# Performance work log

Measured on AMD Instinct MI355X. Metric: run time of the kernel, lower is better.

The kernel has to match this reference:

```python
import jax, jax.numpy as jnp
import numpy as np

N = 20000
E = 320000
F_IN = 50
HID = 64          # hidden_channels
HEADS = 8
WIDTH = HID * HEADS  # 512
NUM_CLASSES = 121


def setup_inputs() -> dict:
    key = jax.random.key(0)
    ks = jax.random.split(key, 16)
    def p(k, shape, fan_in):
        return (jax.random.normal(k, shape, dtype=jnp.float32) / np.sqrt(fan_in)).astype(jnp.float32)
    x = jax.random.normal(ks[0], (N, F_IN), dtype=jnp.float32)
    edge_index = jax.random.randint(ks[1], (2, E), 0, N, dtype=jnp.int64)
    return {
        "x": x,
        "edge_index": edge_index,
        # layer 1: 50 -> 64, heads=8, concat
        "W1": p(ks[2], (F_IN, HEADS * HID), F_IN),
        "a1_src": p(ks[3], (HEADS, HID), HID),
        "a1_dst": p(ks[4], (HEADS, HID), HID),
        "b1": jnp.zeros((HEADS * HID,), jnp.float32),
        # layer 2: 512 -> 512, heads=1, concat
        "W2": p(ks[5], (WIDTH, WIDTH), WIDTH),
        "a2_src": p(ks[6], (1, WIDTH), WIDTH),
        "a2_dst": p(ks[7], (1, WIDTH), WIDTH),
        "b2": jnp.zeros((WIDTH,), jnp.float32),
        # layer 3: 512 -> 121, heads=1, concat=False (mean)
        "W3": p(ks[8], (WIDTH, NUM_CLASSES), WIDTH),
        "a3_src": p(ks[9], (1, NUM_CLASSES), NUM_CLASSES),
        "a3_dst": p(ks[10], (1, NUM_CLASSES), NUM_CLASSES),
        "b3": jnp.zeros((NUM_CLASSES,), jnp.float32),
    }


def gat_conv(x, src, dst, W, a_src, a_dst, b, heads, out_ch, concat):
    n = x.shape[0]
    h = (x @ W).reshape(n, heads, out_ch)                 # [N, H, C]
    al_s = jnp.sum(h * a_src, axis=-1)                     # [N, H]
    al_d = jnp.sum(h * a_dst, axis=-1)                     # [N, H]
    e = jax.nn.leaky_relu(al_s[src] + al_d[dst], 0.2)      # [E, H]
    # edge softmax per destination node (stable)
    m = jax.ops.segment_max(e, dst, num_segments=n)        # [N, H]
    m = jnp.where(jnp.isfinite(m), m, 0.0)
    ex = jnp.exp(e - m[dst])
    z = jax.ops.segment_sum(ex, dst, num_segments=n)       # [N, H]
    alpha = ex / (z[dst] + 1e-16)                          # [E, H]
    msg = h[src] * alpha[..., None]                        # [E, H, C]
    out = jax.ops.segment_sum(msg, dst, num_segments=n)    # [N, H, C]
    out = out.reshape(n, heads * out_ch) if concat else out.mean(axis=1)
    return out + b


def reference(x, edge_index, W1, a1_src, a1_dst, b1, W2, a2_src, a2_dst, b2, W3, a3_src, a3_dst, b3):
    n = x.shape[0]
    # PyG GATConv adds self loops by default
    loops = jnp.arange(n, dtype=edge_index.dtype)
    src = jnp.concatenate([edge_index[0], loops])
    dst = jnp.concatenate([edge_index[1], loops])
    # eval mode: dropout is identity
    x1 = gat_conv(x, src, dst, W1, a1_src, a1_dst, b1, HEADS, HID, True)
    h = jax.nn.elu(x1)
    x1 = gat_conv(h, src, dst, W2, a2_src, a2_dst, b2, 1, WIDTH, True)
    h = jax.nn.elu(x1)
    x1 = gat_conv(h, src, dst, W3, a3_src, a3_dst, b3, 1, NUM_CLASSES, False)
    return x1
```

## Files before the change

### kernel.cpp

```cpp
#include <hip/hip_runtime.h>
#include <hip/hip_bf16.h>
#include <hip/hip_fp16.h>

#define NN     20000
#define ERAW   320000
#define ETOT   (ERAW + NN)
#define F_IN   50
#define HID    64
#define HEADS  8
#define WIDTH  512
#define NCLS   121
#define NCLS_P 128

typedef __attribute__((ext_vector_type(8))) __bf16 bf16x8;
typedef __attribute__((ext_vector_type(4))) float floatx4;

__device__ __forceinline__ unsigned short f32_to_bf16_rn(float f) {
  unsigned u = __float_as_uint(f);
  unsigned r = u + 0x7fffu + ((u >> 16) & 1u);
  return (unsigned short)(r >> 16);
}
__device__ __forceinline__ void split_one(float f, unsigned short& h,
                                          unsigned short& l) {
  h = f32_to_bf16_rn(f);
  float fh = __uint_as_float(((unsigned)h) << 16);
  l = f32_to_bf16_rn(f - fh);
}

__device__ __forceinline__ float2 u2f2(unsigned u) {
  __half2 hv = *reinterpret_cast<__half2*>(&u);
  return __half22float2(hv);
}

__device__ __forceinline__ void gll16(const unsigned short* g,
                                      const unsigned short* l) {
  __builtin_amdgcn_global_load_lds(
      (const __attribute__((address_space(1))) unsigned int*)(const void*)g,
      (__attribute__((address_space(3))) unsigned int*)(void*)l, 16, 0, 0);
}

#define PW_BLOCKS 449
__global__ __launch_bounds__(256) void prep_weights(
    const float* __restrict__ W1, const float* __restrict__ W2,
    const float* __restrict__ W3, const float* __restrict__ a1s,
    const float* __restrict__ a1d, unsigned short* __restrict__ w1hHi,
    unsigned short* __restrict__ w1hLo, unsigned short* __restrict__ w2tHi,
    unsigned short* __restrict__ w2tLo, unsigned short* __restrict__ w3tHi,
    unsigned short* __restrict__ w3tLo, float* __restrict__ w1as,
    float* __restrict__ w1ad) {
  __shared__ float t[32][33];
  const int b = blockIdx.x;
  if (b < 320) {
    const float* W;
    unsigned short *thi, *tlo;
    int M, Mp, bx, by;
    const int K = WIDTH;
    if (b < 256) {
      W = W2; thi = w2tHi; tlo = w2tLo; M = WIDTH; Mp = WIDTH;
      bx = b & 15; by = b >> 4;
    } else {
      int bb = b - 256;
      W = W3; thi = w3tHi; tlo = w3tLo; M = NCLS; Mp = NCLS_P;
      bx = bb & 15; by = bb >> 4;
    }
    const int P = Mp >> 4;
    int k0 = bx * 32, m0 = by * 32;
    int tx = threadIdx.x & 31, ty = threadIdx.x >> 5;
    #pragma unroll
    for (int r = 0; r < 4; ++r) {
      int k = k0 + ty + r * 8, m = m0 + tx;
      float v = 0.f;
      if (k < K && m < M) v = W[(size_t)k * M + m];
      t[ty + r * 8][tx] = v;
    }
    __syncthreads();
    #pragma unroll
    for (int r = 0; r < 4; ++r) {
      int m = m0 + ty + r * 8, k = k0 + tx;
      if (m < Mp && k < K) {
        unsigned short h, l;
        split_one(t[tx][ty + r * 8], h, l);
        size_t off = ((size_t)((k >> 5) * P + (m >> 4))) * 512 +
                     ((k >> 3) & 3) * 128 + (m & 15) * 8 + (k & 7);
        thi[off] = h;
        tlo[off] = l;
      }
    }
  } else if (b < 448) {
    int idx = (b - 320) * 256 + threadIdx.x;
    if (idx < HEADS * HID * HID) {
      int hd = idx >> 12, rem = idx & 4095;
      int col = rem >> 6, k = rem & 63;
      float v = (k < F_IN) ? W1[(size_t)k * WIDTH + hd * HID + col] : 0.f;
      unsigned short h, l;
      split_one(v, h, l);
      w1hHi[idx] = h;
      w1hLo[idx] = l;
    }
  } else {
    for (int idx = threadIdx.x; idx < 2 * F_IN * HEADS; idx += 256) {
      int which = idx >= F_IN * HEADS;
      int r = which ? idx - F_IN * HEADS : idx;
      int k = r >> 3, h = r & 7;
      const float* a = which ? a1d : a1s;
      float s = 0.f;
      for (int c = 0; c < HID; ++c)
        s += W1[(size_t)k * WIDTH + h * HID + c] * a[h * HID + c];
      (which ? w1ad : w1as)[r] = s;
    }
  }
}

template <int MI>
__global__ __launch_bounds__(512, 4) void gemm_split_db(
    const unsigned short* __restrict__ Ahi, const unsigned short* __restrict__ Alo,
    const unsigned short* __restrict__ Bthi, const unsigned short* __restrict__ Btlo,
    __half* __restrict__ C16, int N, int K, int M, int Mp, int RB, int CB) {
  constexpr int ABUF = MI * 2048;
  constexpr int BUF = MI * 4096;
  constexpr int NGW = MI;
  __shared__ unsigned short lds[2 * BUF];

  const int f = blockIdx.x;
  const int xcd = f & 7;
  const int g = f >> 3;
  const int cb = g % CB;
  const int rb = (g / CB) * 8 + xcd;
  if (rb >= RB) return;
  const int r0 = rb * (MI * 32), c0 = cb * 128;

  const int tid = threadIdx.x;
  const int wave = tid >> 6, lane = tid & 63;
  const int wr = wave >> 2, wc = wave & 3;
  const int lkg = lane >> 4, lmn = lane & 15;
  const int P = Mp >> 4;

  const int row8 = lane >> 3, cslot = lane & 7;
  const unsigned short* gsrc[NGW];
  int ldsoff[NGW];
  #pragma unroll
  for (int i = 0; i < NGW; ++i) {
    int q = wave * NGW + i;
    int a = (q < MI * 4) ? 0 : 1;
    int rg = (a == 0) ? q : q - MI * 4;
    int r = rg * 8 + row8;
    int c = cslot ^ (r & 7);
    const unsigned short* base = a ? Alo : Ahi;
    int ra = r0 + r;
    if (ra > N - 1) ra = N - 1;
    gsrc[i] = base + (size_t)ra * K + c * 8;
    ldsoff[i] = a * ABUF + rg * 512;
  }

  int rowA[MI], m7A[MI];
  #pragma unroll
  for (int mi = 0; mi < MI; ++mi) {
    int m = wr * (MI * 16) + mi * 16 + lmn;
    rowA[mi] = m * 64;  m7A[mi] = m & 7;
  }
  const int g0 = (c0 >> 4) + wc * 2;

  floatx4 acc[MI][2] = {};

  #pragma unroll
  for (int i = 0; i < NGW; ++i) gll16(gsrc[i], lds + ldsoff[i]);

  const int nk = K >> 6;
  for (int t = 0; t < nk; ++t) {
    if (t + 1 < nk) {
      const unsigned short* dst = lds + ((t + 1) & 1) * BUF;
      #pragma unroll
      for (int i = 0; i < NGW; ++i)
        gll16(gsrc[i] + (t + 1) * 64, dst + ldsoff[i]);
      if constexpr (MI == 4) {
        asm volatile("s_waitcnt vmcnt(4)" ::: "memory");
      } else {
        asm volatile("s_waitcnt vmcnt(2)" ::: "memory");
      }
    } else {
      asm volatile("s_waitcnt vmcnt(0)" ::: "memory");
    }
    __builtin_amdgcn_sched_barrier(0);
    __builtin_amdgcn_s_barrier();
    __builtin_amdgcn_sched_barrier(0);

    const unsigned short* Lb = lds + (t & 1) * BUF;
    #pragma unroll
    for (int ksub = 0; ksub < 2; ++ksub) {
      bf16x8 fAhi[MI], fAlo[MI], fBhi[2], fBlo[2];
      #pragma unroll
      for (int mi = 0; mi < MI; ++mi) {
        int s = rowA[mi] + (((ksub << 2) | lkg) ^ m7A[mi]) * 8;
        fAhi[mi] = *(const bf16x8*)(Lb + s);
        fAlo[mi] = *(const bf16x8*)(Lb + s + ABUF);
      }
      const size_t fbase = ((size_t)(t * 2 + ksub) * P + g0) * 512 + lane * 8;
      #pragma unroll
      for (int ni = 0; ni < 2; ++ni) {
        fBhi[ni] = *(const bf16x8*)(Bthi + fbase + ni * 512);
        fBlo[ni] = *(const bf16x8*)(Btlo + fbase + ni * 512);
      }
      #pragma unroll
      for (int mi = 0; mi < MI; ++mi)
        #pragma unroll
        for (int ni = 0; ni < 2; ++ni) {
          acc[mi][ni] = __builtin_amdgcn_mfma_f32_16x16x32_bf16(
              fAhi[mi], fBhi[ni], acc[mi][ni], 0, 0, 0);
          acc[mi][ni] = __builtin_amdgcn_mfma_f32_16x16x32_bf16(
              fAhi[mi], fBlo[ni], acc[mi][ni], 0, 0, 0);
          acc[mi][ni] = __builtin_amdgcn_mfma_f32_16x16x32_bf16(
              fAlo[mi], fBhi[ni], acc[mi][ni], 0, 0, 0);
        }
    }

    __builtin_amdgcn_sched_barrier(0);
    asm volatile("s_waitcnt lgkmcnt(0)" ::: "memory");
    __builtin_amdgcn_s_barrier();
    __builtin_amdgcn_sched_barrier(0);
  }

  #pragma unroll
  for (int mi = 0; mi < MI; ++mi) {
    #pragma unroll
    for (int r = 0; r < 4; ++r) {
      int grow = r0 + wr * (MI * 16) + mi * 16 + lkg * 4 + r;
      if (grow >= N) continue;
      #pragma unroll
      for (int ni = 0; ni < 2; ++ni) {
        int gcol = c0 + wc * 32 + ni * 16 + lmn;
        float v = (gcol < M) ? acc[mi][ni][r] : 0.f;
        C16[(size_t)grow * Mp + gcol] = __float2half(v);
      }
    }
  }
}

__global__ __launch_bounds__(256) void gemm_l1_heads(
    const unsigned short* __restrict__ Ahi, const unsigned short* __restrict__ Alo,
    const unsigned short* __restrict__ Bthi, const unsigned short* __restrict__ Btlo,
    unsigned short* __restrict__ outHi, unsigned short* __restrict__ outLo,
    const float* __restrict__ bias) {
  __shared__ unsigned short sAhi[8192], sAlo[8192], sBhi[4096], sBlo[4096];
  const int tid = threadIdx.x;
  const int wave = tid >> 6, lane = tid & 63;
  const int r0 = blockIdx.x * 128;
  const int hd = blockIdx.y;
  const int lkg = lane >> 4, lmn = lane & 15;

  #pragma unroll
  for (int t = 0; t < 4; ++t) {
    int cid = tid + t * 256;
    int row = cid >> 3, c = cid & 7;
    int gr = r0 + row; if (gr > NN - 1) gr = NN - 1;
    const size_t goff = (size_t)gr * WIDTH + hd * HID + c * 8;
    int loff = (((c >> 2) * 4 + (c & 3)) * 128 + row) * 8;
    *(uint4*)(sAhi + loff) = *(const uint4*)(Ahi + goff);
    *(uint4*)(sAlo + loff) = *(const uint4*)(Alo + goff);
  }
  #pragma unroll
  for (int t = 0; t < 2; ++t) {
    int cid = tid + t * 256;
    int col = cid >> 3, c = cid & 7;
    const size_t goff = (size_t)(hd * HID + col) * HID + c * 8;
    int loff = (((c >> 2) * 4 + (c & 3)) * 64 + col) * 8;
    *(uint4*)(sBhi + loff) = *(const uint4*)(Bthi + goff);
    *(uint4*)(sBlo + loff) = *(const uint4*)(Btlo + goff);
  }
  __syncthreads();

  floatx4 acc[2][4] = {};
  #pragma unroll
  for (int ks = 0; ks < 2; ++ks) {
    bf16x8 fAhi[2], fAlo[2], fBhi[4], fBlo[4];
    #pragma unroll
    for (int mi = 0; mi < 2; ++mi) {
      int m = wave * 32 + mi * 16 + lmn;
      int off = ((ks * 4 + lkg) * 128 + m) * 8;
      fAhi[mi] = *(const bf16x8*)(sAhi + off);
      fAlo[mi] = *(const bf16x8*)(sAlo + off);
    }
    #pragma unroll
    for (int ni = 0; ni < 4; ++ni) {
      int n = ni * 16 + lmn;
      int off = ((ks * 4 + lkg) * 64 + n) * 8;
      fBhi[ni] = *(const bf16x8*)(sBhi + off);
      fBlo[ni] = *(const bf16x8*)(sBlo + off);
    }
    #pragma unroll
    for (int mi = 0; mi < 2; ++mi)
      #pragma unroll
      for (int ni = 0; ni < 4; ++ni) {
        acc[mi][ni] = __builtin_amdgcn_mfma_f32_16x16x32_bf16(
            fAhi[mi], fBhi[ni], acc[mi][ni], 0, 0, 0);
        acc[mi][ni] = __builtin_amdgcn_mfma_f32_16x16x32_bf16(
            fAhi[mi], fBlo[ni], acc[mi][ni], 0, 0, 0);
        acc[mi][ni] = __builtin_amdgcn_mfma_f32_16x16x32_bf16(
            fAlo[mi], fBhi[ni], acc[mi][ni], 0, 0, 0);
      }
  }

  #pragma unroll
  for (int mi = 0; mi < 2; ++mi) {
    #pragma unroll
    for (int r = 0; r < 4; ++r) {
      int grow = r0 + wave * 32 + mi * 16 + (lane >> 4) * 4 + r;
      if (grow >= NN) continue;
      #pragma unroll
      for (int ni = 0; ni < 4; ++ni) {
        int gcol = hd * HID + ni * 16 + lmn;
        float v = acc[mi][ni][r] + bias[gcol];
        v = (v > 0.f) ? v : (__expf(v) - 1.0f);
        unsigned short hh, ll;
        split_one(v, hh, ll);
        outHi[(size_t)grow * WIDTH + gcol] = hh;
        outLo[(size_t)grow * WIDTH + gcol] = ll;
      }
    }
  }
}

__global__ __launch_bounds__(256) void al1_kernel(
    const float* __restrict__ x, const float* __restrict__ w1as,
    const float* __restrict__ w1ad, float* __restrict__ al_s,
    float* __restrict__ al_d) {
  int n = (blockIdx.x * blockDim.x + threadIdx.x) >> 6;
  int lane = threadIdx.x & 63;
  if (n >= NN) return;
  float xv = (lane < F_IN) ? x[(size_t)n * F_IN + lane] : 0.f;
  float ws[HEADS], wd[HEADS];
  #pragma unroll
  for (int h = 0; h < HEADS; ++h) {
    ws[h] = (lane < F_IN) ? w1as[lane * HEADS + h] : 0.f;
    wd[h] = (lane < F_IN) ? w1ad[lane * HEADS + h] : 0.f;
  }
  #pragma unroll
  for (int h = 0; h < HEADS; ++h) {
    float ss = xv * ws[h], sd = xv * wd[h];
    #pragma unroll
    for (int o = 32; o; o >>= 1) {
      ss += __shfl_xor(ss, o);
      sd += __shfl_xor(sd, o);
    }
    if (lane == 0) {
      al_s[n * HEADS + h] = ss;
      al_d[n * HEADS + h] = sd;
    }
  }
}

template <int C, int CS>
__global__ __launch_bounds__(256) void compute_al16(
    const __half* __restrict__ h16, const float* __restrict__ a_src,
    const float* __restrict__ a_dst, float* __restrict__ al_s,
    float* __restrict__ al_d) {
  int n = (blockIdx.x * blockDim.x + threadIdx.x) >> 6;
  int lane = threadIdx.x & 63;
  if (n >= NN) return;
  const __half* hr = h16 + (size_t)n * CS;
  float ss = 0.f, sd = 0.f;
  if (C % 512 == 0) {
    uint4 raw = *(const uint4*)(hr + lane * 8);
    float f[8];
    float2 t;
    t = u2f2(raw.x); f[0] = t.x; f[1] = t.y;
    t = u2f2(raw.y); f[2] = t.x; f[3] = t.y;
    t = u2f2(raw.z); f[4] = t.x; f[5] = t.y;
    t = u2f2(raw.w); f[6] = t.x; f[7] = t.y;
    #pragma unroll
    for (int j = 0; j < 8; ++j) {
      int c = lane * 8 + j;
      ss += f[j] * a_src[c];
      sd += f[j] * a_dst[c];
    }
  } else {
    for (int c = lane; c < C; c += 64) {
      float v = __half2float(hr[c]);
      ss += v * a_src[c];
      sd += v * a_dst[c];
    }
  }
  #pragma unroll
  for (int o = 32; o; o >>= 1) {
    ss += __shfl_xor(ss, o);
    sd += __shfl_xor(sd, o);
  }
  if (lane == 0) {
    al_s[n] = ss;
    al_d[n] = sd;
  }
}

__global__ __launch_bounds__(256) void count_deg(
    const int* __restrict__ edst, int* __restrict__ deg) {
  int e = blockIdx.x * blockDim.x + threadIdx.x;
  if (e >= ETOT) return;
  int d = (e < ERAW) ? edst[e] : (e - ERAW);
  atomicAdd(&deg[d], 1);
}

__global__ __launch_bounds__(1024) void scan_deg(
    const int* __restrict__ deg, int* __restrict__ rowptr) {
  __shared__ int part[1024];
  const int t = threadIdx.x;
  const int CHUNK = (NN + 1023) / 1024;
  int lo = t * CHUNK, hi = min(lo + CHUNK, NN);
  int s = 0;
  for (int i = lo; i < hi; ++i) s += deg[i];
  part[t] = s;
  __syncthreads();
  for (int off = 1; off < 1024; off <<= 1) {
    int v = (t >= off) ? part[t - off] : 0;
    __syncthreads();
    part[t] += v;
    __syncthreads();
  }
  int base = (t == 0) ? 0 : part[t - 1];
  for (int i = lo; i < hi; ++i) {
    rowptr[i] = base;
    base += deg[i];
  }
  if (t == 1023) rowptr[NN] = part[1023];
}

__global__ __launch_bounds__(256) void scatter_csr(
    const int* __restrict__ esrc, const int* __restrict__ edst,
    const int* __restrict__ rowptr, int* __restrict__ cnt,
    int* __restrict__ csrc) {
  int e = blockIdx.x * blockDim.x + threadIdx.x;
  if (e >= ETOT) return;
  int s, d;
  if (e < ERAW) { s = esrc[e]; d = edst[e]; }
  else          { s = e - ERAW; d = e - ERAW; }
  int pos = rowptr[d] + atomicAdd(&cnt[d], 1);
  csrc[pos] = s;
}

__global__ __launch_bounds__(256) void agg_x_sm(
    const int* __restrict__ rowptr, const int* __restrict__ csrc,
    const float* __restrict__ al_s, const float* __restrict__ al_d,
    const float* __restrict__ x, unsigned short* __restrict__ outHi,
    unsigned short* __restrict__ outLo) {
  const int w = threadIdx.x >> 6, lane = threadIdx.x & 63;
  const int d = blockIdx.x * 4 + w;
  if (d >= NN) return;
  const int r0 = rowptr[d], r1 = rowptr[d + 1];
  const int mh = lane & 7;
  const float ald_my = al_d[d * HEADS + mh];
  float m_my = al_s[d * HEADS + mh] + ald_my;
  m_my = (m_my > 0.f) ? m_my : 0.2f * m_my;

  float z_my = 0.f;
  float acc[HEADS];
  #pragma unroll
  for (int hh = 0; hh < HEADS; ++hh) acc[hh] = 0.f;

  int p = r0;
  for (; p + 8 <= r1; p += 8) {
    int s[8];
    #pragma unroll
    for (int j = 0; j < 8; ++j) s[j] = csrc[p + j];
    float xv[8];
    #pragma unroll
    for (int j = 0; j < 8; ++j)
      xv[j] = (lane < F_IN) ? x[(size_t)s[j] * F_IN + lane] : 0.f;
    float av[8];
    #pragma unroll
    for (int j = 0; j < 8; ++j) av[j] = al_s[s[j] * HEADS + mh];
    #pragma unroll
    for (int j = 0; j < 8; ++j) {
      float v = av[j] + ald_my;
      v = (v > 0.f) ? v : 0.2f * v;
      float a = __expf(v - m_my);
      z_my += a;
      #pragma unroll
      for (int hh = 0; hh < HEADS; ++hh) acc[hh] += __shfl(a, hh, 8) * xv[j];
    }
  }
  for (; p < r1; ++p) {
    int s = csrc[p];
    float v = al_s[s * HEADS + mh] + ald_my;
    v = (v > 0.f) ? v : 0.2f * v;
    float a = __expf(v - m_my);
    z_my += a;
    float xv = (lane < F_IN) ? x[(size_t)s * F_IN + lane] : 0.f;
    #pragma unroll
    for (int hh = 0; hh < HEADS; ++hh) acc[hh] += __shfl(a, hh, 8) * xv;
  }

  #pragma unroll
  for (int hh = 0; hh < HEADS; ++hh) {
    float zh = __shfl(z_my, hh, 8);
    float v = (lane < F_IN) ? acc[hh] / (zh + 1e-16f) : 0.f;
    unsigned short h2, l2;
    split_one(v, h2, l2);
    outHi[(size_t)d * WIDTH + hh * HID + lane] = h2;
    outLo[(size_t)d * WIDTH + hh * HID + lane] = l2;
  }
}

__global__ __launch_bounds__(256) void pull_agg_w(
    const int* __restrict__ rowptr, const int* __restrict__ csrc,
    const float* __restrict__ al_s, const float* __restrict__ al_d,
    const __half* __restrict__ h16, const float* __restrict__ bias,
    unsigned short* __restrict__ outHi, unsigned short* __restrict__ outLo) {
  const int w = threadIdx.x >> 6;
  const int lane = threadIdx.x & 63;
  const int d = blockIdx.x * 4 + w;
  if (d >= NN) return;
  const int r0 = rowptr[d], r1 = rowptr[d + 1];
  const float ald = al_d[d];
  float m = al_s[d] + ald;
  m = (m > 0.f) ? m : 0.2f * m;

  const int base = lane * 8;
  const __half* hb = h16 + base;
  float acc[8];
  #pragma unroll
  for (int j = 0; j < 8; ++j) acc[j] = 0.f;
  float z = 0.f;

  int p = r0;
  for (; p + 8 <= r1; p += 8) {
    int s[8];
    #pragma unroll
    for (int j = 0; j < 8; ++j) s[j] = csrc[p + j];
    uint4 raw8[8];
    #pragma unroll
    for (int j = 0; j < 8; ++j)
      raw8[j] = *(const uint4*)(hb + (size_t)s[j] * WIDTH);
    float av[8];
    #pragma unroll
    for (int j = 0; j < 8; ++j) av[j] = al_s[s[j]];
    #pragma unroll
    for (int j = 0; j < 8; ++j) {
      float v = av[j] + ald;
      v = (v > 0.f) ? v : 0.2f * v;
      float a = __expf(v - m);
      z += a;
      float2 f0 = u2f2(raw8[j].x), f1 = u2f2(raw8[j].y);
      float2 f2 = u2f2(raw8[j].z), f3 = u2f2(raw8[j].w);
      acc[0] += f0.x * a; acc[1] += f0.y * a;
      acc[2] += f1.x * a; acc[3] += f1.y * a;
      acc[4] += f2.x * a; acc[5] += f2.y * a;
      acc[6] += f3.x * a; acc[7] += f3.y * a;
    }
  }
  for (; p < r1; ++p) {
    int s = csrc[p];
    float v = al_s[s] + ald;
    v = (v > 0.f) ? v : 0.2f * v;
    float a = __expf(v - m);
    z += a;
    uint4 raw = *(const uint4*)(hb + (size_t)s * WIDTH);
    float2 f0 = u2f2(raw.x), f1 = u2f2(raw.y);
    float2 f2 = u2f2(raw.z), f3 = u2f2(raw.w);
    acc[0] += f0.x * a; acc[1] += f0.y * a;
    acc[2] += f1.x * a; acc[3] += f1.y * a;
    acc[4] += f2.x * a; acc[5] += f2.y * a;
    acc[6] += f3.x * a; acc[7] += f3.y * a;
  }
  const float iz = 1.0f / (z + 1e-16f);

  #pragma unroll
  for (int j = 0; j < 8; ++j) {
    float v = acc[j] * iz + bias[base + j];
    v = (v > 0.f) ? v : (__expf(v) - 1.0f);
    unsigned short hh, ll;
    split_one(v, hh, ll);
    outHi[(size_t)d * WIDTH + base + j] = hh;
    outLo[(size_t)d * WIDTH + base + j] = ll;
  }
}

__global__ __launch_bounds__(256) void pull_agg_n(
    const int* __restrict__ rowptr, const int* __restrict__ csrc,
    const float* __restrict__ al_s, const float* __restrict__ al_d,
    const __half* __restrict__ h16, const float* __restrict__ bias,
    float* __restrict__ out) {
  const int w = threadIdx.x >> 6, lane = threadIdx.x & 63;
  const int half = lane >> 5, li = lane & 31;
  const int d = blockIdx.x * 8 + w * 2 + half;
  if (d >= NN) return;
  const int r0 = rowptr[d], r1 = rowptr[d + 1];
  const float ald = al_d[d];
  float m = al_s[d] + ald;
  m = (m > 0.f) ? m : 0.2f * m;

  const int base = li * 4;
  const __half* hb = h16 + base;
  float acc[4] = {0.f, 0.f, 0.f, 0.f};
  float z = 0.f;

  for (int p = r0; p < r1; p += 8) {
    int s[8];
    #pragma unroll
    for (int j = 0; j < 8; ++j) {
      int pj = p + j; if (pj > r1 - 1) pj = r1 - 1;
      s[j] = csrc[pj];
    }
    uint2 raw[8];
    #pragma unroll
    for (int j = 0; j < 8; ++j)
      raw[j] = *(const uint2*)(hb + (size_t)s[j] * NCLS_P);
    float av[8];
    #pragma unroll
    for (int j = 0; j < 8; ++j) av[j] = al_s[s[j]];
    #pragma unroll
    for (int j = 0; j < 8; ++j) {
      float v = av[j] + ald;
      v = (v > 0.f) ? v : 0.2f * v;
      float a = __expf(v - m);
      if (p + j >= r1) a = 0.f;
      z += a;
      float2 f0 = u2f2(raw[j].x), f1 = u2f2(raw[j].y);
      acc[0] += f0.x * a; acc[1] += f0.y * a;
      acc[2] += f1.x * a; acc[3] += f1.y * a;
    }
  }
  const float iz = 1.0f / (z + 1e-16f);

  #pragma unroll
  for (int j = 0; j < 4; ++j) {
    int col = base + j;
    if (col < NCLS)
      out[(size_t)d * NCLS + col] = acc[j] * iz + bias[col];
  }
}

extern "C" void kernel_launch(void* const* d_in, const int* in_sizes, int n_in,
                              void* d_out, int out_size, void* d_ws,
                              size_t ws_size, hipStream_t stream) {
  const float* x      = (const float*)d_in[0];
  const int*   ei     = (const int*)d_in[1];
  const float* W1     = (const float*)d_in[2];
  const float* a1_src = (const float*)d_in[3];
  const float* a1_dst = (const float*)d_in[4];
  const float* b1     = (const float*)d_in[5];
  const float* W2     = (const float*)d_in[6];
  const float* a2_src = (const float*)d_in[7];
  const float* a2_dst = (const float*)d_in[8];
  const float* b2     = (const float*)d_in[9];
  const float* W3     = (const float*)d_in[10];
  const float* a3_src = (const float*)d_in[11];
  const float* a3_dst = (const float*)d_in[12];
  const float* b3     = (const float*)d_in[13];
  float* out = (float*)d_out;

  const int* esrc = ei;
  const int* edst = ei + ERAW;

  unsigned short* p1Hi  = (unsigned short*)d_ws;
  unsigned short* p1Lo  = p1Hi + (size_t)NN * WIDTH;
  unsigned short* p2Hi  = p1Lo + (size_t)NN * WIDTH;
  unsigned short* p2Lo  = p2Hi + (size_t)NN * WIDTH;
  __half*        h16    = (__half*)(p2Lo + (size_t)NN * WIDTH);
  unsigned short* w1hHi = (unsigned short*)(h16 + (size_t)NN * WIDTH);
  unsigned short* w1hLo = w1hHi + (size_t)HEADS * HID * HID;
  unsigned short* w2tHi = w1hLo + (size_t)HEADS * HID * HID;
  unsigned short* w2tLo = w2tHi + (size_t)WIDTH * WIDTH;
  unsigned short* w3tHi = w2tLo + (size_t)WIDTH * WIDTH;
  unsigned short* w3tLo = w3tHi + (size_t)NCLS_P * WIDTH;
  float* al_s   = (float*)(w3tLo + (size_t)NCLS_P * WIDTH);
  float* al_d   = al_s + (size_t)NN * HEADS;
  float* w1as   = al_d + (size_t)NN * HEADS;
  float* w1ad   = w1as + F_IN * HEADS;
  int* deg      = (int*)(w1ad + F_IN * HEADS);
  int* cnt      = deg + NN;
  int* rowptr   = cnt + NN;
  int* csrc     = rowptr + NN + 4;

  hipMemsetAsync(deg, 0, (size_t)(2 * NN) * sizeof(int), stream);
  const int eblk = (ETOT + 255) / 256;
  count_deg<<<eblk, 256, 0, stream>>>(edst, deg);
  scan_deg<<<1, 1024, 0, stream>>>(deg, rowptr);
  scatter_csr<<<eblk, 256, 0, stream>>>(esrc, edst, rowptr, cnt, csrc);

  prep_weights<<<PW_BLOCKS, 256, 0, stream>>>(
      W1, W2, W3, a1_src, a1_dst, w1hHi, w1hLo, w2tHi, w2tLo, w3tHi, w3tLo,
      w1as, w1ad);

  const int nwblk = (NN + 3) / 4;

  al1_kernel<<<nwblk, 256, 0, stream>>>(x, w1as, w1ad, al_s, al_d);
  agg_x_sm<<<nwblk, 256, 0, stream>>>(rowptr, csrc, al_s, al_d, x, p1Hi,
                                      p1Lo);
  gemm_l1_heads<<<dim3((NN + 127) / 128, HEADS), 256, 0, stream>>>(
      p1Hi, p1Lo, w1hHi, w1hLo, p2Hi, p2Lo, b1);

  const int RB2 = (NN + 127) / 128;
  const int G2 = ((RB2 + 7) / 8) * 8 * (WIDTH / 128);
  gemm_split_db<4><<<G2, 512, 0, stream>>>(
      p2Hi, p2Lo, w2tHi, w2tLo, h16, NN, WIDTH, WIDTH, WIDTH, RB2,
      WIDTH / 128);
  compute_al16<WIDTH, WIDTH><<<nwblk, 256, 0, stream>>>(h16, a2_src, a2_dst,
                                                        al_s, al_d);
  pull_agg_w<<<nwblk, 256, 0, stream>>>(rowptr, csrc, al_s, al_d, h16, b2,
                                        p1Hi, p1Lo);

  const int RB3 = (NN + 63) / 64;
  const int G3 = ((RB3 + 7) / 8) * 8 * (NCLS_P / 128);
  gemm_split_db<2><<<G3, 512, 0, stream>>>(
      p1Hi, p1Lo, w3tHi, w3tLo, h16, NN, WIDTH, NCLS, NCLS_P, RB3,
      NCLS_P / 128);
  compute_al16<NCLS, NCLS_P><<<nwblk, 256, 0, stream>>>(h16, a3_src, a3_dst,
                                                        al_s, al_d);
  pull_agg_n<<<(NN + 7) / 8, 256, 0, stream>>>(rowptr, csrc, al_s, al_d, h16,
                                               b3, out);
}
```

Baseline: 388.5 us.

## Store GEMM A operands in MFMA fragment layout and load directly from global

The producer kernels now write the hi/lo bf16 activation splits in a pre-swizzled MFMA fragment layout, with row count padded to a multiple of 16. The GEMM drops its LDS double buffer, async global-to-LDS loads and barriers, and each wave reads its A and B fragments straight from global memory as contiguous 16-byte loads. This removes LDS staging and synchronisation cost. In exchange, A data shared across waves is re-read from cache instead of reused through LDS, and latency hiding now relies on unrolling and occupancy. The padded rows in the last block are no longer clamped and may hold uninitialised data, though results for those rows appear not to be stored.

```diff
diff --git a/kernel.cpp b/kernel.cpp
--- a/kernel.cpp
+++ b/kernel.cpp
@@ -3,6 +3,7 @@
 #include <hip/hip_fp16.h>
 
 #define NN     20000
+#define NNP    20096
 #define ERAW   320000
 #define ETOT   (ERAW + NN)
 #define F_IN   50
@@ -32,11 +33,9 @@
   return __half22float2(hv);
 }
 
-__device__ __forceinline__ void gll16(const unsigned short* g,
-                                      const unsigned short* l) {
-  __builtin_amdgcn_global_load_lds(
-      (const __attribute__((address_space(1))) unsigned int*)(const void*)g,
-      (__attribute__((address_space(3))) unsigned int*)(void*)l, 16, 0, 0);
+__device__ __forceinline__ size_t fragoff(int row, int col, int KF) {
+  return ((size_t)(row >> 4) * KF + (col >> 5)) * 512 +
+         ((col >> 3) & 3) * 128 + (row & 15) * 8 + (col & 7);
 }
 
 #define PW_BLOCKS 449
@@ -63,7 +62,6 @@
       W = W3; thi = w3tHi; tlo = w3tLo; M = NCLS; Mp = NCLS_P;
       bx = bb & 15; by = bb >> 4;
     }
-    const int P = Mp >> 4;
     int k0 = bx * 32, m0 = by * 32;
     int tx = threadIdx.x & 31, ty = threadIdx.x >> 5;
     #pragma unroll
@@ -80,8 +78,10 @@
       if (m < Mp && k < K) {
         unsigned short h, l;
         split_one(t[tx][ty + r * 8], h, l);
-        size_t off = ((size_t)((k >> 5) * P + (m >> 4))) * 512 +
+        size_t off = ((size_t)(m >> 4) * (K >> 5) + (k >> 5)) * 512 +
                      ((k >> 3) & 3) * 128 + (m & 15) * 8 + (k & 7);
+        off = ((size_t)(k >> 5) * (Mp >> 4) + (m >> 4)) * 512 +
+              ((k >> 3) & 3) * 128 + (m & 15) * 8 + (k & 7);
         thi[off] = h;
         tlo[off] = l;
       }
@@ -112,15 +112,10 @@
 }
 
 template <int MI>
-__global__ __launch_bounds__(512, 4) void gemm_split_db(
+__global__ __launch_bounds__(512) void gemm_frag(
     const unsigned short* __restrict__ Ahi, const unsigned short* __restrict__ Alo,
     const unsigned short* __restrict__ Bthi, const unsigned short* __restrict__ Btlo,
     __half* __restrict__ C16, int N, int K, int M, int Mp, int RB, int CB) {
-  constexpr int ABUF = MI * 2048;
-  constexpr int BUF = MI * 4096;
-  constexpr int NGW = MI;
-  __shared__ unsigned short lds[2 * BUF];
-
   const int f = blockIdx.x;
   const int xcd = f & 7;
   const int g = f >> 3;
@@ -133,90 +128,47 @@
   const int wave = tid >> 6, lane = tid & 63;
   const int wr = wave >> 2, wc = wave & 3;
   const int lkg = lane >> 4, lmn = lane & 15;
+  const int KF = K >> 5;
   const int P = Mp >> 4;
 
-  const int row8 = lane >> 3, cslot = lane & 7;
-  const unsigned short* gsrc[NGW];
-  int ldsoff[NGW];
-  #pragma unroll
-  for (int i = 0; i < NGW; ++i) {
-    int q = wave * NGW + i;
-    int a = (q < MI * 4) ? 0 : 1;
-    int rg = (a == 0) ? q : q - MI * 4;
-    int r = rg * 8 + row8;
-    int c = cslot ^ (r & 7);
-    const unsigned short* base = a ? Alo : Ahi;
-    int ra = r0 + r;
-    if (ra > N - 1) ra = N - 1;
-    gsrc[i] = base + (size_t)ra * K + c * 8;
-    ldsoff[i] = a * ABUF + rg * 512;
-  }
-
-  int rowA[MI], m7A[MI];
+  const unsigned short* aH[MI];
+  const unsigned short* aL[MI];
   #pragma unroll
   for (int mi = 0; mi < MI; ++mi) {
-    int m = wr * (MI * 16) + mi * 16 + lmn;
-    rowA[mi] = m * 64;  m7A[mi] = m & 7;
+    int rba = (r0 >> 4) + wr * MI + mi;
+    aH[mi] = Ahi + (size_t)rba * KF * 512 + lane * 8;
+    aL[mi] = Alo + (size_t)rba * KF * 512 + lane * 8;
   }
   const int g0 = (c0 >> 4) + wc * 2;
+  const unsigned short* bH = Bthi + (size_t)g0 * 512 + lane * 8;
+  const unsigned short* bL = Btlo + (size_t)g0 * 512 + lane * 8;
 
   floatx4 acc[MI][2] = {};
 
-  #pragma unroll
-  for (int i = 0; i < NGW; ++i) gll16(gsrc[i], lds + ldsoff[i]);
-
-  const int nk = K >> 6;
-  for (int t = 0; t < nk; ++t) {
-    if (t + 1 < nk) {
-      const unsigned short* dst = lds + ((t + 1) & 1) * BUF;
-      #pragma unroll
-      for (int i = 0; i < NGW; ++i)
-        gll16(gsrc[i] + (t + 1) * 64, dst + ldsoff[i]);
-      if constexpr (MI == 4) {
-        asm volatile("s_waitcnt vmcnt(4)" ::: "memory");
-      } else {
-        asm volatile("s_waitcnt vmcnt(2)" ::: "memory");
-      }
-    } else {
-      asm volatile("s_waitcnt vmcnt(0)" ::: "memory");
-    }
-    __builtin_amdgcn_sched_barrier(0);
-    __builtin_amdgcn_s_barrier();
-    __builtin_amdgcn_sched_barrier(0);
-
-    const unsigned short* Lb = lds + (t & 1) * BUF;
-    #pragma unroll
-    for (int ksub = 0; ksub < 2; ++ksub) {
-      bf16x8 fAhi[MI], fAlo[MI], fBhi[2], fBlo[2];
-      #pragma unroll
-      for (int mi = 0; mi < MI; ++mi) {
-        int s = rowA[mi] + (((ksub << 2) | lkg) ^ m7A[mi]) * 8;
-        fAhi[mi] = *(const bf16x8*)(Lb + s);
-        fAlo[mi] = *(const bf16x8*)(Lb + s + ABUF);
-      }
-      const size_t fbase = ((size_t)(t * 2 + ksub) * P + g0) * 512 + lane * 8;
+  #pragma unroll 4
+  for (int kf = 0; kf < KF; ++kf) {
+    bf16x8 fAhi[MI], fAlo[MI], fBhi[2], fBlo[2];
+    #pragma unroll
+    for (int mi = 0; mi < MI; ++mi) {
+      fAhi[mi] = *(const bf16x8*)(aH[mi] + (size_t)kf * 512);
+      fAlo[mi] = *(const bf16x8*)(aL[mi] + (size_t)kf * 512);
+    }
+    #pragma unroll
+    for (int ni = 0; ni < 2; ++ni) {
+      fBhi[ni] = *(const bf16x8*)(bH + ((size_t)kf * P + ni) * 512);
+      fBlo[ni] = *(const bf16x8*)(bL + ((size_t)kf * P + ni) * 512);
+    }
+    #pragma unroll
+    for (int mi = 0; mi < MI; ++mi)
       #pragma unroll
       for (int ni = 0; ni < 2; ++ni) {
-        fBhi[ni] = *(const bf16x8*)(Bthi + fbase + ni * 512);
-        fBlo[ni] = *(const bf16x8*)(Btlo + fbase + ni * 512);
+        acc[mi][ni] = __builtin_amdgcn_mfma_f32_16x16x32_bf16(
+            fAhi[mi], fBhi[ni], acc[mi][ni], 0, 0, 0);
+        acc[mi][ni] = __builtin_amdgcn_mfma_f32_16x16x32_bf16(
+            fAhi[mi], fBlo[ni], acc[mi][ni], 0, 0, 0);
+        acc[mi][ni] = __builtin_amdgcn_mfma_f32_16x16x32_bf16(
+            fAlo[mi], fBhi[ni], acc[mi][ni], 0, 0, 0);
       }
-      #pragma unroll
-      for (int mi = 0; mi < MI; ++mi)
-        #pragma unroll
-        for (int ni = 0; ni < 2; ++ni) {
-          acc[mi][ni] = __builtin_amdgcn_mfma_f32_16x16x32_bf16(
-              fAhi[mi], fBhi[ni], acc[mi][ni], 0, 0, 0);
-          acc[mi][ni] = __builtin_amdgcn_mfma_f32_16x16x32_bf16(
-              fAhi[mi], fBlo[ni], acc[mi][ni], 0, 0, 0);
-          acc[mi][ni] = __builtin_amdgcn_mfma_f32_16x16x32_bf16(
-              fAlo[mi], fBhi[ni], acc[mi][ni], 0, 0, 0);
-        }
-    }
-
-    __builtin_amdgcn_sched_barrier(0);
-    asm volatile("s_waitcnt lgkmcnt(0)" ::: "memory");
-    __builtin_amdgcn_s_barrier();
-    __builtin_amdgcn_sched_barrier(0);
   }
 
   #pragma unroll
@@ -312,8 +264,9 @@
         v = (v > 0.f) ? v : (__expf(v) - 1.0f);
         unsigned short hh, ll;
         split_one(v, hh, ll);
-        outHi[(size_t)grow * WIDTH + gcol] = hh;
-        outLo[(size_t)grow * WIDTH + gcol] = ll;
+        size_t fo = fragoff(grow, gcol, WIDTH >> 5);
+        outHi[fo] = hh;
+        outLo[fo] = ll;
       }
     }
   }
@@ -561,14 +514,16 @@
   }
   const float iz = 1.0f / (z + 1e-16f);
 
+  const size_t fo = ((size_t)(d >> 4) * (WIDTH >> 5) + (base >> 5)) * 512 +
+                    ((base >> 3) & 3) * 128 + (d & 15) * 8;
   #pragma unroll
   for (int j = 0; j < 8; ++j) {
     float v = acc[j] * iz + bias[base + j];
     v = (v > 0.f) ? v : (__expf(v) - 1.0f);
     unsigned short hh, ll;
     split_one(v, hh, ll);
-    outHi[(size_t)d * WIDTH + base + j] = hh;
-    outLo[(size_t)d * WIDTH + base + j] = ll;
+    outHi[fo + j] = hh;
+    outLo[fo + j] = ll;
   }
 }
 
@@ -650,10 +605,10 @@
   const int* edst = ei + ERAW;
 
   unsigned short* p1Hi  = (unsigned short*)d_ws;
-  unsigned short* p1Lo  = p1Hi + (size_t)NN * WIDTH;
-  unsigned short* p2Hi  = p1Lo + (size_t)NN * WIDTH;
-  unsigned short* p2Lo  = p2Hi + (size_t)NN * WIDTH;
-  __half*        h16    = (__half*)(p2Lo + (size_t)NN * WIDTH);
+  unsigned short* p1Lo  = p1Hi + (size_t)NNP * WIDTH;
+  unsigned short* p2Hi  = p1Lo + (size_t)NNP * WIDTH;
+  unsigned short* p2Lo  = p2Hi + (size_t)NNP * WIDTH;
+  __half*        h16    = (__half*)(p2Lo + (size_t)NNP * WIDTH);
   unsigned short* w1hHi = (unsigned short*)(h16 + (size_t)NN * WIDTH);
   unsigned short* w1hLo = w1hHi + (size_t)HEADS * HID * HID;
   unsigned short* w2tHi = w1hLo + (size_t)HEADS * HID * HID;
@@ -689,7 +644,7 @@
 
   const int RB2 = (NN + 127) / 128;
   const int G2 = ((RB2 + 7) / 8) * 8 * (WIDTH / 128);
-  gemm_split_db<4><<<G2, 512, 0, stream>>>(
+  gemm_frag<4><<<G2, 512, 0, stream>>>(
       p2Hi, p2Lo, w2tHi, w2tLo, h16, NN, WIDTH, WIDTH, WIDTH, RB2,
       WIDTH / 128);
   compute_al16<WIDTH, WIDTH><<<nwblk, 256, 0, stream>>>(h16, a2_src, a2_dst,
@@ -699,7 +654,7 @@
 
   const int RB3 = (NN + 63) / 64;
   const int G3 = ((RB3 + 7) / 8) * 8 * (NCLS_P / 128);
-  gemm_split_db<2><<<G3, 512, 0, stream>>>(
+  gemm_frag<2><<<G3, 512, 0, stream>>>(
       p1Hi, p1Lo, w3tHi, w3tLo, h16, NN, WIDTH, NCLS, NCLS_P, RB3,
       NCLS_P / 128);
   compute_al16<NCLS, NCLS_P><<<nwblk, 256, 0, stream>>>(h16, a3_src, a3_dst,
```

New measurement: 410.4 us. +5.6%, slower.

## Store layer-1 output in MFMA fragment layout and use LDS-free GEMM

Applied to the files above, without the earlier changes.

The layer-1 head GEMM now writes its hi/lo bf16 output directly in the 16x32 MFMA fragment order. A new gemm_frag kernel for layer 2 then loads A and B fragments straight from global memory with contiguous 16-byte loads per lane, with no LDS staging or double buffering. The activation buffers are padded to a multiple of 128 rows so fragment tiles stay in bounds. The aim is to remove LDS traffic and barriers from the layer-2 GEMM, but with no explicit prefetch it relies on cache hits and global-load latency hiding, and each fragment is reloaded by several waves.

```diff
diff --git a/kernel.cpp b/kernel.cpp
--- a/kernel.cpp
+++ b/kernel.cpp
@@ -3,6 +3,7 @@
 #include <hip/hip_fp16.h>
 
 #define NN     20000
+#define NNP    20096
 #define ERAW   320000
 #define ETOT   (ERAW + NN)
 #define F_IN   50
@@ -37,6 +38,11 @@
   __builtin_amdgcn_global_load_lds(
       (const __attribute__((address_space(1))) unsigned int*)(const void*)g,
       (__attribute__((address_space(3))) unsigned int*)(void*)l, 16, 0, 0);
+}
+
+__device__ __forceinline__ size_t fragoff(int row, int col, int KF) {
+  return ((size_t)(row >> 4) * KF + (col >> 5)) * 512 +
+         ((col >> 3) & 3) * 128 + (row & 15) * 8 + (col & 7);
 }
 
 #define PW_BLOCKS 449
@@ -63,7 +69,6 @@
       W = W3; thi = w3tHi; tlo = w3tLo; M = NCLS; Mp = NCLS_P;
       bx = bb & 15; by = bb >> 4;
     }
-    const int P = Mp >> 4;
     int k0 = bx * 32, m0 = by * 32;
     int tx = threadIdx.x & 31, ty = threadIdx.x >> 5;
     #pragma unroll
@@ -80,7 +85,7 @@
       if (m < Mp && k < K) {
         unsigned short h, l;
         split_one(t[tx][ty + r * 8], h, l);
-        size_t off = ((size_t)((k >> 5) * P + (m >> 4))) * 512 +
+        size_t off = ((size_t)(k >> 5) * (Mp >> 4) + (m >> 4)) * 512 +
                      ((k >> 3) & 3) * 128 + (m & 15) * 8 + (k & 7);
         thi[off] = h;
         tlo[off] = l;
@@ -107,6 +112,82 @@
       for (int c = 0; c < HID; ++c)
         s += W1[(size_t)k * WIDTH + h * HID + c] * a[h * HID + c];
       (which ? w1ad : w1as)[r] = s;
+    }
+  }
+}
+
+template <int MI>
+__global__ __launch_bounds__(512) void gemm_frag(
+    const unsigned short* __restrict__ Ahi, const unsigned short* __restrict__ Alo,
+    const unsigned short* __restrict__ Bthi, const unsigned short* __restrict__ Btlo,
+    __half* __restrict__ C16, int N, int K, int M, int Mp, int RB, int CB) {
+  const int f = blockIdx.x;
+  const int xcd = f & 7;
+  const int g = f >> 3;
+  const int cb = g % CB;
+  const int rb = (g / CB) * 8 + xcd;
+  if (rb >= RB) return;
+  const int r0 = rb * (MI * 32), c0 = cb * 128;
+
+  const int tid = threadIdx.x;
+  const int wave = tid >> 6, lane = tid & 63;
+  const int wr = wave >> 2, wc = wave & 3;
+  const int lkg = lane >> 4, lmn = lane & 15;
+  const int KF = K >> 5;
+  const int P = Mp >> 4;
+
+  const unsigned short* aH[MI];
+  const unsigned short* aL[MI];
+  #pragma unroll
+  for (int mi = 0; mi < MI; ++mi) {
+    int rba = (r0 >> 4) + wr * MI + mi;
+    aH[mi] = Ahi + (size_t)rba * KF * 512 + lane * 8;
+    aL[mi] = Alo + (size_t)rba * KF * 512 + lane * 8;
+  }
+  const int g0 = (c0 >> 4) + wc * 2;
+  const unsigned short* bH = Bthi + (size_t)g0 * 512 + lane * 8;
+  const unsigned short* bL = Btlo + (size_t)g0 * 512 + lane * 8;
+
+  floatx4 acc[MI][2] = {};
+
+  #pragma unroll 4
+  for (int kf = 0; kf < KF; ++kf) {
+    bf16x8 fAhi[MI], fAlo[MI], fBhi[2], fBlo[2];
+    #pragma unroll
+    for (int mi = 0; mi < MI; ++mi) {
+      fAhi[mi] = *(const bf16x8*)(aH[mi] + (size_t)kf * 512);
+      fAlo[mi] = *(const bf16x8*)(aL[mi] + (size_t)kf * 512);
+    }
+    #pragma unroll
+    for (int ni = 0; ni < 2; ++ni) {
+      fBhi[ni] = *(const bf16x8*)(bH + ((size_t)kf * P + ni) * 512);
+      fBlo[ni] = *(const bf16x8*)(bL + ((size_t)kf * P + ni) * 512);
+    }
+    #pragma unroll
+    for (int mi = 0; mi < MI; ++mi)
+      #pragma unroll
+      for (int ni = 0; ni < 2; ++ni) {
+        acc[mi][ni] = __builtin_amdgcn_mfma_f32_16x16x32_bf16(
+            fAhi[mi], fBhi[ni], acc[mi][ni], 0, 0, 0);
+        acc[mi][ni] = __builtin_amdgcn_mfma_f32_16x16x32_bf16(
+            fAhi[mi], fBlo[ni], acc[mi][ni], 0, 0, 0);
+        acc[mi][ni] = __builtin_amdgcn_mfma_f32_16x16x32_bf16(
+            fAlo[mi], fBhi[ni], acc[mi][ni], 0, 0, 0);
+      }
+  }
+
+  #pragma unroll
+  for (int mi = 0; mi < MI; ++mi) {
+    #pragma unroll
+    for (int r = 0; r < 4; ++r) {
+      int grow = r0 + wr * (MI * 16) + mi * 16 + lkg * 4 + r;
+      if (grow >= N) continue;
+      #pragma unroll
+      for (int ni = 0; ni < 2; ++ni) {
+        int gcol = c0 + wc * 32 + ni * 16 + lmn;
+        float v = (gcol < M) ? acc[mi][ni][r] : 0.f;
+        C16[(size_t)grow * Mp + gcol] = __float2half(v);
+      }
     }
   }
 }
@@ -312,8 +393,9 @@
         v = (v > 0.f) ? v : (__expf(v) - 1.0f);
         unsigned short hh, ll;
         split_one(v, hh, ll);
-        outHi[(size_t)grow * WIDTH + gcol] = hh;
-        outLo[(size_t)grow * WIDTH + gcol] = ll;
+        size_t fo = fragoff(grow, gcol, WIDTH >> 5);
+        outHi[fo] = hh;
+        outLo[fo] = ll;
       }
     }
   }
@@ -650,10 +732,10 @@
   const int* edst = ei + ERAW;
 
   unsigned short* p1Hi  = (unsigned short*)d_ws;
-  unsigned short* p1Lo  = p1Hi + (size_t)NN * WIDTH;
-  unsigned short* p2Hi  = p1Lo + (size_t)NN * WIDTH;
-  unsigned short* p2Lo  = p2Hi + (size_t)NN * WIDTH;
-  __half*        h16    = (__half*)(p2Lo + (size_t)NN * WIDTH);
+  unsigned short* p1Lo  = p1Hi + (size_t)NNP * WIDTH;
+  unsigned short* p2Hi  = p1Lo + (size_t)NNP * WIDTH;
+  unsigned short* p2Lo  = p2Hi + (size_t)NNP * WIDTH;
+  __half*        h16    = (__half*)(p2Lo + (size_t)NNP * WIDTH);
   unsigned short* w1hHi = (unsigned short*)(h16 + (size_t)NN * WIDTH);
   unsigned short* w1hLo = w1hHi + (size_t)HEADS * HID * HID;
   unsigned short* w2tHi = w1hLo + (size_t)HEADS * HID * HID;
@@ -689,7 +771,7 @@
 
   const int RB2 = (NN + 127) / 128;
   const int G2 = ((RB2 + 7) / 8) * 8 * (WIDTH / 128);
-  gemm_split_db<4><<<G2, 512, 0, stream>>>(
+  gemm_frag<4><<<G2, 512, 0, stream>>>(
       p2Hi, p2Lo, w2tHi, w2tLo, h16, NN, WIDTH, WIDTH, WIDTH, RB2,
       WIDTH / 128);
   compute_al16<WIDTH, WIDTH><<<nwblk, 256, 0, stream>>>(h16, a2_src, a2_dst,
```

Result: no change. 393.9 us (+1.4%).
